# Optimization experiments

Measured on AMD Instinct MI355X. Metric: run time of the kernel, lower is better.

The kernel has to match this reference:

```python
import jax, jax.numpy as jnp
import numpy as np

N_NODES = 50000
N_EDGES = 600000
EMBED_DIM = 128


def setup_inputs() -> dict:
    key = jax.random.key(0)
    k1, k2 = jax.random.split(key)
    x = jax.random.normal(k1, (N_NODES, EMBED_DIM), dtype=jnp.float32)
    edge_index = jax.random.randint(k2, (2, N_EDGES), 0, N_NODES, dtype=jnp.int64)
    bias = jnp.zeros((EMBED_DIM,), dtype=jnp.float32)
    return {"x": x, "edge_index": edge_index, "bias": bias}


def reference(x, edge_index, bias):
    # init_embedding is Identity (disable_init_embedding=True)
    init_embeds = x
    n = x.shape[0]
    # add_self_loops
    loops = jnp.arange(n, dtype=edge_index.dtype)
    row = jnp.concatenate([edge_index[0], loops])  # source nodes
    col = jnp.concatenate([edge_index[1], loops])  # destination nodes
    # degree of destination nodes
    deg = jax.ops.segment_sum(jnp.ones_like(col, dtype=x.dtype), col, num_segments=n)
    deg_inv_sqrt = jnp.where(deg > 0, jax.lax.rsqrt(jnp.maximum(deg, 1e-20)), 0.0)
    # symmetric GCN normalization per edge
    norm = deg_inv_sqrt[row] * deg_inv_sqrt[col]  # [E+N]
    # message: gather source features, scale, scatter-add into destinations
    msg = norm[:, None] * x[row]  # [E+N, D]
    out = jax.ops.segment_sum(msg, col, num_segments=n) + bias
    return (out, init_embeds)
```

## Files before the change

### kernel.cpp

```cpp
#include <hip/hip_runtime.h>

#define D 128
#define B 256
#define WMAX 64
#define SPILL_MAX 8192
#define NPART 8
#define PLACE_BLOCKS 2048

typedef float vfloat4 __attribute__((ext_vector_type(4)));


__device__ __forceinline__ unsigned short f2bf(float f) {
    unsigned u = __float_as_uint(f);
    u = u + 0x7FFFu + ((u >> 16) & 1u);
    return (unsigned short)(u >> 16);
}

__device__ __forceinline__ vfloat4 bf2f4(unsigned lo, unsigned hi) {
    vfloat4 r;
    r.x = __uint_as_float(lo << 16);
    r.y = __uint_as_float(lo & 0xffff0000u);
    r.z = __uint_as_float(hi << 16);
    r.w = __uint_as_float(hi & 0xffff0000u);
    return r;
}

__global__ void k_zero2(int* __restrict__ cursor, int* __restrict__ spillCnt, int n) {
    int i = blockIdx.x * blockDim.x + threadIdx.x;
    if (i == 0) *spillCnt = 0;
    if (i < n) cursor[i] = 0;
}

__global__ void k_mega(const float* __restrict__ x, float* __restrict__ out2,
                       uint2* __restrict__ xb,
                       const int* __restrict__ row, const int* __restrict__ col,
                       int* __restrict__ cursor, int* __restrict__ ssrc,
                       int2* __restrict__ spill, int* __restrict__ spillCnt,
                       int e, int n) {
    int bid = blockIdx.x;
    int t   = threadIdx.x;

    if (bid < PLACE_BLOCKS) {
        int p  = bid & (NPART - 1);
        int bg = bid >> 3;
        int tg = bg * B + t;
        int T  = (PLACE_BLOCKS >> 3) * B;
        int lo = (int)((long long)n * p / NPART);
        int hi = (int)((long long)n * (p + 1) / NPART);

        for (int i = tg; i < e; i += T) {
            int c = col[i];
            if (c < lo || c >= hi) continue;
            int r = row[i];
            int pos = atomicAdd(&cursor[c], 1);
            if (pos < WMAX) {
                ssrc[c * WMAX + pos] = r;
            } else {
                int s = atomicAdd(spillCnt, 1);
                if (s < SPILL_MAX) spill[s] = make_int2(r, c);
            }
        }
    } else {
        int gid = (bid - PLACE_BLOCKS) * B + t;
        if (gid >= n * 32) return;
        vfloat4 xv = reinterpret_cast<const vfloat4*>(x)[gid];
        __builtin_nontemporal_store(xv, reinterpret_cast<vfloat4*>(out2) + gid);
        uint2 b;
        b.x = (unsigned)f2bf(xv.x) | ((unsigned)f2bf(xv.y) << 16);
        b.y = (unsigned)f2bf(xv.z) | ((unsigned)f2bf(xv.w) << 16);
        xb[gid] = b;
    }
}

__global__ void k_agg_ell(const uint2* __restrict__ xb, const float* __restrict__ bias,
                          const int* __restrict__ cursor, const int* __restrict__ ssrc,
                          const int2* __restrict__ spill, const int* __restrict__ spillCnt,
                          float* __restrict__ out, int n) {
    int p  = blockIdx.x & (NPART - 1);
    int bg = blockIdx.x >> 3;
    int lo = (int)((long long)n * p / NPART);
    int hi = (int)((long long)n * (p + 1) / NPART);
    int node = lo + bg * 8 + (threadIdx.x >> 5);
    if (node >= hi) return;
    int q = threadIdx.x & 31;

    int cnt = cursor[node];
    int m   = min(cnt, WMAX);
    const int* sp = ssrc + node * WMAX;

    vfloat4 a0 = {0.f, 0.f, 0.f, 0.f};
    vfloat4 a1 = a0, a2 = a0, a3 = a0;

    int j = 0;
    for (; j + 4 <= m; j += 4) {
        int r0 = sp[j + 0], r1 = sp[j + 1], r2 = sp[j + 2], r3 = sp[j + 3];
        uint2 v0 = xb[(size_t)r0 * 32 + q];
        uint2 v1 = xb[(size_t)r1 * 32 + q];
        uint2 v2 = xb[(size_t)r2 * 32 + q];
        uint2 v3 = xb[(size_t)r3 * 32 + q];
        float w0 = rsqrtf((float)cursor[r0] + 1.0f);
        float w1 = rsqrtf((float)cursor[r1] + 1.0f);
        float w2 = rsqrtf((float)cursor[r2] + 1.0f);
        float w3 = rsqrtf((float)cursor[r3] + 1.0f);
        a0 += w0 * bf2f4(v0.x, v0.y);
        a1 += w1 * bf2f4(v1.x, v1.y);
        a2 += w2 * bf2f4(v2.x, v2.y);
        a3 += w3 * bf2f4(v3.x, v3.y);
    }
    for (; j < m; ++j) {
        int r = sp[j];
        uint2 v = xb[(size_t)r * 32 + q];
        float w = rsqrtf((float)cursor[r] + 1.0f);
        a0 += w * bf2f4(v.x, v.y);
    }

    if (cnt > WMAX) {
        int sc = min(*spillCnt, SPILL_MAX);
        for (int s = 0; s < sc; ++s) {
            int2 pr = spill[s];
            if (pr.y == node) {
                float w = rsqrtf((float)cursor[pr.x] + 1.0f);
                uint2 v = xb[(size_t)pr.x * 32 + q];
                a0 += w * bf2f4(v.x, v.y);
            }
        }
    }

    float dc = rsqrtf((float)cnt + 1.0f);
    uint2 xc2 = xb[(size_t)node * 32 + q];
    vfloat4 xc = bf2f4(xc2.x, xc2.y);
    vfloat4 bv = reinterpret_cast<const vfloat4*>(bias)[q];
    vfloat4 ov = bv + dc * (a0 + a1 + a2 + a3 + dc * xc);

    __builtin_nontemporal_store(ov, reinterpret_cast<vfloat4*>(out) + (size_t)node * 32 + q);
}


__global__ void k_zero(int* __restrict__ degInt, int n) {
    int i = blockIdx.x * blockDim.x + threadIdx.x;
    if (i < n) degInt[i] = 0;
}

__global__ void k_count(const int* __restrict__ col, int* __restrict__ degInt, int e) {
    int i = blockIdx.x * blockDim.x + threadIdx.x;
    if (i < e) atomicAdd(&degInt[col[i]], 1);
}

__global__ void k_scan1(const int* __restrict__ degInt, int* __restrict__ off,
                        int* __restrict__ bsum, int n) {
    __shared__ int sm[B];
    int i = blockIdx.x * B + threadIdx.x;
    int v = (i < n) ? degInt[i] : 0;
    sm[threadIdx.x] = v;
    __syncthreads();
    for (int s = 1; s < B; s <<= 1) {
        int t = (threadIdx.x >= (unsigned)s) ? sm[threadIdx.x - s] : 0;
        __syncthreads();
        sm[threadIdx.x] += t;
        __syncthreads();
    }
    if (i < n) off[i] = sm[threadIdx.x] - v;
    if (threadIdx.x == B - 1) bsum[blockIdx.x] = sm[B - 1];
}

__global__ void k_scan2(int* __restrict__ bsum, int nb) {
    __shared__ int sm[B];
    int v = (threadIdx.x < (unsigned)nb) ? bsum[threadIdx.x] : 0;
    sm[threadIdx.x] = v;
    __syncthreads();
    for (int s = 1; s < B; s <<= 1) {
        int t = (threadIdx.x >= (unsigned)s) ? sm[threadIdx.x - s] : 0;
        __syncthreads();
        sm[threadIdx.x] += t;
        __syncthreads();
    }
    if (threadIdx.x < (unsigned)nb) bsum[threadIdx.x] = sm[threadIdx.x] - v;
}

__global__ void k_scan3(int* __restrict__ off, const int* __restrict__ bsum,
                        const int* __restrict__ degInt, float* __restrict__ dis,
                        int* __restrict__ cursor, int n, int e) {
    int i = blockIdx.x * B + threadIdx.x;
    if (i < n) {
        int o = off[i] + bsum[blockIdx.x];
        off[i] = o;
        cursor[i] = o;
        dis[i] = rsqrtf((float)degInt[i] + 1.0f);
    }
    if (i == 0) off[n] = e;
}

__global__ void k_place_pairs(const int* __restrict__ row, const int* __restrict__ col,
                              const float* __restrict__ dis, int* __restrict__ cursor,
                              int2* __restrict__ pairs, int e) {
    int i = blockIdx.x * blockDim.x + threadIdx.x;
    if (i >= e) return;
    int r = row[i];
    int c = col[i];
    float w = dis[r];
    int pos = atomicAdd(&cursor[c], 1);
    pairs[pos] = make_int2(r, __float_as_int(w));
}

__global__ void k_aggregate_pairs(const float* __restrict__ x, const float* __restrict__ bias,
                                  const float* __restrict__ dis, const int* __restrict__ off,
                                  const int2* __restrict__ pairs, float* __restrict__ out,
                                  float* __restrict__ out2, int n) {
    int gid = blockIdx.x * blockDim.x + threadIdx.x;
    if (gid >= n * 32) return;
    int node = gid >> 5;
    int q    = gid & 31;
    const vfloat4* x4 = reinterpret_cast<const vfloat4*>(x);
    int j   = off[node];
    int end = off[node + 1];
    vfloat4 a0 = {0.f, 0.f, 0.f, 0.f};
    vfloat4 a1 = a0, a2 = a0, a3 = a0;
    for (; j + 4 <= end; j += 4) {
        int2 p0 = pairs[j + 0];
        int2 p1 = pairs[j + 1];
        int2 p2 = pairs[j + 2];
        int2 p3 = pairs[j + 3];
        vfloat4 v0 = x4[(size_t)p0.x * 32 + q];
        vfloat4 v1 = x4[(size_t)p1.x * 32 + q];
        vfloat4 v2 = x4[(size_t)p2.x * 32 + q];
        vfloat4 v3 = x4[(size_t)p3.x * 32 + q];
        a0 += __int_as_float(p0.y) * v0;
        a1 += __int_as_float(p1.y) * v1;
        a2 += __int_as_float(p2.y) * v2;
        a3 += __int_as_float(p3.y) * v3;
    }
    for (; j < end; ++j) {
        int2 p = pairs[j];
        a0 += __int_as_float(p.y) * x4[(size_t)p.x * 32 + q];
    }
    float dc = dis[node];
    vfloat4 xc = x4[(size_t)node * 32 + q];
    vfloat4 bv = reinterpret_cast<const vfloat4*>(bias)[q];
    vfloat4 ov = bv + dc * (a0 + a1 + a2 + a3 + dc * xc);
    __builtin_nontemporal_store(ov, reinterpret_cast<vfloat4*>(out)  + (size_t)node * 32 + q);
    __builtin_nontemporal_store(xc, reinterpret_cast<vfloat4*>(out2) + (size_t)node * 32 + q);
}


extern "C" void kernel_launch(void* const* d_in, const int* in_sizes, int n_in,
                              void* d_out, int out_size, void* d_ws, size_t ws_size,
                              hipStream_t stream) {
    const float* x    = (const float*)d_in[0];
    const int*   idx  = (const int*)d_in[1];
    const float* bias = (const float*)d_in[2];

    const int n = in_sizes[0] / D;
    const int e = in_sizes[1] / 2;

    const int* row = idx;
    const int* col = idx + e;

    float* out  = (float*)d_out;
    float* out2 = (float*)d_out + (size_t)n * D;

    const int nbN  = (n + B - 1) / B;
    const int nbE  = (e + B - 1) / B;
    const int prepB = (n * 32 + B - 1) / B;

    char* p0 = (char*)d_ws;
    int*  cursor  = (int*)p0;                        p0 += (size_t)n * 4;
    int*  spillCnt= (int*)p0;                        p0 += 16;
    int2* spill   = (int2*)p0;                       p0 += (size_t)SPILL_MAX * 8;
    p0 = (char*)(((uintptr_t)p0 + 15) & ~(uintptr_t)15);
    uint2* xb     = (uint2*)p0;                      p0 += (size_t)n * 32 * 8;
    int*  ssrc    = (int*)p0;                        p0 += (size_t)n * WMAX * 4;
    size_t need_ell = (size_t)(p0 - (char*)d_ws);

    if (ws_size >= need_ell) {
        int maxPart = 0;
        for (int p = 0; p < NPART; ++p) {
            int lo = (int)((long long)n * p / NPART);
            int hi = (int)((long long)n * (p + 1) / NPART);
            if (hi - lo > maxPart) maxPart = hi - lo;
        }
        const int bpg = (maxPart + 7) / 8;
        const int agB = bpg * NPART;
        const int megaB = PLACE_BLOCKS + prepB;

        k_zero2  <<<nbN,   B, 0, stream>>>(cursor, spillCnt, n);
        k_mega   <<<megaB, B, 0, stream>>>(x, out2, xb, row, col, cursor, ssrc,
                                           spill, spillCnt, e, n);
        k_agg_ell<<<agB,   B, 0, stream>>>(xb, bias, cursor, ssrc, spill, spillCnt, out, n);
        return;
    }

    char* p = (char*)d_ws;
    int*   degInt = (int*)p;            p += (size_t)n * 4;
    int*   cur2   = (int*)p;            p += (size_t)n * 4;
    int*   off    = (int*)p;            p += (size_t)(n + 1) * 4;
    int*   bsum   = (int*)p;            p += 256 * 4;
    float* dis    = (float*)p;          p += (size_t)n * 4;
    p = (char*)(((uintptr_t)p + 15) & ~(uintptr_t)15);
    int2*  pairs  = (int2*)p;

    const int aggB = (n * 32 + B - 1) / B;
    k_zero <<<nbN, B, 0, stream>>>(degInt, n);
    k_count<<<nbE, B, 0, stream>>>(col, degInt, e);
    k_scan1<<<nbN, B, 0, stream>>>(degInt, off, bsum, n);
    k_scan2<<<1,   B, 0, stream>>>(bsum, nbN);
    k_scan3<<<nbN, B, 0, stream>>>(off, bsum, degInt, dis, cur2, n, e);
    k_place_pairs<<<nbE, B, 0, stream>>>(row, col, dis, cur2, pairs, e);
    k_aggregate_pairs<<<aggB, B, 0, stream>>>(x, bias, dis, off, pairs, out, out2, n);
}
```

Measured before the change: 78.99 us.

## Fold cursor zeroing into prep kernel, split placement, unroll aggregation by eight

The cursor/spill-counter zeroing moves into the bf16 conversion and copy kernel. Edge placement becomes its own kernel, so it no longer shares a launch with the conversion work. This keeps the same three-launch count but changes which work overlaps: placement can no longer run concurrently with the conversion. The aggregation loop is also unrolled to eight neighbours per iteration to put more gathers in flight, which costs more registers.

```diff
diff --git a/kernel.cpp b/kernel.cpp
--- a/kernel.cpp
+++ b/kernel.cpp
@@ -5,7 +5,6 @@
 #define WMAX 64
 #define SPILL_MAX 8192
 #define NPART 8
-#define PLACE_BLOCKS 2048
 
 typedef float vfloat4 __attribute__((ext_vector_type(4)));
 
@@ -25,50 +24,43 @@
     return r;
 }
 
-__global__ void k_zero2(int* __restrict__ cursor, int* __restrict__ spillCnt, int n) {
-    int i = blockIdx.x * blockDim.x + threadIdx.x;
-    if (i == 0) *spillCnt = 0;
-    if (i < n) cursor[i] = 0;
-}
-
-__global__ void k_mega(const float* __restrict__ x, float* __restrict__ out2,
-                       uint2* __restrict__ xb,
-                       const int* __restrict__ row, const int* __restrict__ col,
-                       int* __restrict__ cursor, int* __restrict__ ssrc,
-                       int2* __restrict__ spill, int* __restrict__ spillCnt,
-                       int e, int n) {
-    int bid = blockIdx.x;
-    int t   = threadIdx.x;
-
-    if (bid < PLACE_BLOCKS) {
-        int p  = bid & (NPART - 1);
-        int bg = bid >> 3;
-        int tg = bg * B + t;
-        int T  = (PLACE_BLOCKS >> 3) * B;
-        int lo = (int)((long long)n * p / NPART);
-        int hi = (int)((long long)n * (p + 1) / NPART);
-
-        for (int i = tg; i < e; i += T) {
-            int c = col[i];
-            if (c < lo || c >= hi) continue;
-            int r = row[i];
-            int pos = atomicAdd(&cursor[c], 1);
-            if (pos < WMAX) {
-                ssrc[c * WMAX + pos] = r;
-            } else {
-                int s = atomicAdd(spillCnt, 1);
-                if (s < SPILL_MAX) spill[s] = make_int2(r, c);
-            }
+__global__ void k_prep(const float* __restrict__ x, float* __restrict__ out2,
+                       uint2* __restrict__ xb, int* __restrict__ cursor,
+                       int* __restrict__ spillCnt, int n) {
+    int gid = blockIdx.x * blockDim.x + threadIdx.x;
+    if (gid == 0) *spillCnt = 0;
+    if (gid < n) cursor[gid] = 0;
+    if (gid >= n * 32) return;
+    vfloat4 xv = reinterpret_cast<const vfloat4*>(x)[gid];
+    __builtin_nontemporal_store(xv, reinterpret_cast<vfloat4*>(out2) + gid);
+    uint2 b;
+    b.x = (unsigned)f2bf(xv.x) | ((unsigned)f2bf(xv.y) << 16);
+    b.y = (unsigned)f2bf(xv.z) | ((unsigned)f2bf(xv.w) << 16);
+    xb[gid] = b;
+}
+
+__global__ void k_place_ell(const int* __restrict__ row, const int* __restrict__ col,
+                            int* __restrict__ cursor, int* __restrict__ ssrc,
+                            int2* __restrict__ spill, int* __restrict__ spillCnt,
+                            int e, int n) {
+    int p  = blockIdx.x & (NPART - 1);
+    int bg = blockIdx.x >> 3;
+    int tg = bg * blockDim.x + threadIdx.x;
+    int T  = (gridDim.x >> 3) * blockDim.x;
+    int lo = (int)((long long)n * p / NPART);
+    int hi = (int)((long long)n * (p + 1) / NPART);
+
+    for (int i = tg; i < e; i += T) {
+        int c = col[i];
+        if (c < lo || c >= hi) continue;
+        int r = row[i];
+        int pos = atomicAdd(&cursor[c], 1);
+        if (pos < WMAX) {
+            ssrc[c * WMAX + pos] = r;
+        } else {
+            int s = atomicAdd(spillCnt, 1);
+            if (s < SPILL_MAX) spill[s] = make_int2(r, c);
         }
-    } else {
-        int gid = (bid - PLACE_BLOCKS) * B + t;
-        if (gid >= n * 32) return;
-        vfloat4 xv = reinterpret_cast<const vfloat4*>(x)[gid];
-        __builtin_nontemporal_store(xv, reinterpret_cast<vfloat4*>(out2) + gid);
-        uint2 b;
-        b.x = (unsigned)f2bf(xv.x) | ((unsigned)f2bf(xv.y) << 16);
-        b.y = (unsigned)f2bf(xv.z) | ((unsigned)f2bf(xv.w) << 16);
-        xb[gid] = b;
     }
 }
 
@@ -92,8 +84,36 @@
     vfloat4 a1 = a0, a2 = a0, a3 = a0;
 
     int j = 0;
+    for (; j + 8 <= m; j += 8) {
+        int r0 = sp[j+0], r1 = sp[j+1], r2 = sp[j+2], r3 = sp[j+3];
+        int r4_ = sp[j+4], r5 = sp[j+5], r6 = sp[j+6], r7 = sp[j+7];
+        uint2 v0 = xb[(size_t)r0 * 32 + q];
+        uint2 v1 = xb[(size_t)r1 * 32 + q];
+        uint2 v2 = xb[(size_t)r2 * 32 + q];
+        uint2 v3 = xb[(size_t)r3 * 32 + q];
+        uint2 v4 = xb[(size_t)r4_ * 32 + q];
+        uint2 v5 = xb[(size_t)r5 * 32 + q];
+        uint2 v6 = xb[(size_t)r6 * 32 + q];
+        uint2 v7 = xb[(size_t)r7 * 32 + q];
+        float w0 = rsqrtf((float)cursor[r0] + 1.0f);
+        float w1 = rsqrtf((float)cursor[r1] + 1.0f);
+        float w2 = rsqrtf((float)cursor[r2] + 1.0f);
+        float w3 = rsqrtf((float)cursor[r3] + 1.0f);
+        float w4 = rsqrtf((float)cursor[r4_] + 1.0f);
+        float w5 = rsqrtf((float)cursor[r5] + 1.0f);
+        float w6 = rsqrtf((float)cursor[r6] + 1.0f);
+        float w7 = rsqrtf((float)cursor[r7] + 1.0f);
+        a0 += w0 * bf2f4(v0.x, v0.y);
+        a1 += w1 * bf2f4(v1.x, v1.y);
+        a2 += w2 * bf2f4(v2.x, v2.y);
+        a3 += w3 * bf2f4(v3.x, v3.y);
+        a0 += w4 * bf2f4(v4.x, v4.y);
+        a1 += w5 * bf2f4(v5.x, v5.y);
+        a2 += w6 * bf2f4(v6.x, v6.y);
+        a3 += w7 * bf2f4(v7.x, v7.y);
+    }
     for (; j + 4 <= m; j += 4) {
-        int r0 = sp[j + 0], r1 = sp[j + 1], r2 = sp[j + 2], r3 = sp[j + 3];
+        int r0 = sp[j+0], r1 = sp[j+1], r2 = sp[j+2], r3 = sp[j+3];
         uint2 v0 = xb[(size_t)r0 * 32 + q];
         uint2 v1 = xb[(size_t)r1 * 32 + q];
         uint2 v2 = xb[(size_t)r2 * 32 + q];
@@ -258,8 +278,8 @@
     float* out  = (float*)d_out;
     float* out2 = (float*)d_out + (size_t)n * D;
 
-    const int nbN  = (n + B - 1) / B;
-    const int nbE  = (e + B - 1) / B;
+    const int nbN = (n + B - 1) / B;
+    const int nbE = (e + B - 1) / B;
     const int prepB = (n * 32 + B - 1) / B;
 
     char* p0 = (char*)d_ws;
@@ -272,6 +292,7 @@
     size_t need_ell = (size_t)(p0 - (char*)d_ws);
 
     if (ws_size >= need_ell) {
+        const int plB = 2048;
         int maxPart = 0;
         for (int p = 0; p < NPART; ++p) {
             int lo = (int)((long long)n * p / NPART);
@@ -280,12 +301,9 @@
         }
         const int bpg = (maxPart + 7) / 8;
         const int agB = bpg * NPART;
-        const int megaB = PLACE_BLOCKS + prepB;
-
-        k_zero2  <<<nbN,   B, 0, stream>>>(cursor, spillCnt, n);
-        k_mega   <<<megaB, B, 0, stream>>>(x, out2, xb, row, col, cursor, ssrc,
-                                           spill, spillCnt, e, n);
-        k_agg_ell<<<agB,   B, 0, stream>>>(xb, bias, cursor, ssrc, spill, spillCnt, out, n);
+        k_prep     <<<prepB, B, 0, stream>>>(x, out2, xb, cursor, spillCnt, n);
+        k_place_ell<<<plB,   B, 0, stream>>>(row, col, cursor, ssrc, spill, spillCnt, e, n);
+        k_agg_ell  <<<agB,   B, 0, stream>>>(xb, bias, cursor, ssrc, spill, spillCnt, out, n);
         return;
     }
 
```

After: 77.57 us. About the same (-1.8%).
